# Performance work log

Measured on AMD Instinct MI355X. Metric: run time of the kernel, lower is better.

The kernel has to match this reference:

```python
import jax, jax.numpy as jnp
import numpy as np

N_NODES = 100_000
N_EDGES = 1_600_000
NFEAT = 16          # nfeature_dim
HID = 128           # hidden_dim
K = 3               # TAGConv hops in pretrained convs
N_LAYERS = 4        # pretrained n_gnn_layers (1 in->hid + 3 hid->hid)
OUT_DIM = 1


def _gcn_norm(edge_index, n):
    # PyG TAGConv: symmetric gcn_norm WITHOUT self-loops (k=0 term covers self).
    row, col = edge_index[0], edge_index[1]
    deg = jax.ops.segment_sum(jnp.ones((edge_index.shape[1],), jnp.float32), col, num_segments=n)
    dis = jnp.where(deg > 0, jax.lax.rsqrt(jnp.maximum(deg, 1.0)), 0.0)
    return dis[row] * dis[col]


def _tagconv(x, row, col, norm, ws, b, n):
    # out = sum_k (A_hat^k x) W_k + b ; ws: [K+1, in, out]
    out = x @ ws[0]
    h = x
    for k in range(1, ws.shape[0]):
        h = jax.ops.segment_sum(h[row] * norm[:, None], col, num_segments=n)
        out = out + h @ ws[k]
    return out + b


def setup_inputs() -> dict:
    key = jax.random.key(0)
    ks = jax.random.split(key, 10)
    x = jax.random.normal(ks[0], (N_NODES, NFEAT + 1), jnp.float32)
    edge_index = jax.random.randint(ks[1], (2, N_EDGES), 0, N_NODES, dtype=jnp.int64)
    # featureEmbedding: TAGConv(17 -> 16, K=1) -> 2 weight mats + bias
    fe_ws = jax.random.normal(ks[2], (2, NFEAT + 1, NFEAT), jnp.float32) * (NFEAT + 1) ** -0.5
    fe_b = jnp.zeros((NFEAT,), jnp.float32)
    # convs[0]: TAGConv(16 -> 128, K=3)
    conv0_ws = jax.random.normal(ks[3], (K + 1, NFEAT, HID), jnp.float32) * NFEAT ** -0.5
    conv0_b = jnp.zeros((HID,), jnp.float32)
    # convs[1..3]: TAGConv(128 -> 128, K=3), stacked
    conv_ws = jax.random.normal(ks[4], (N_LAYERS - 1, K + 1, HID, HID), jnp.float32) * HID ** -0.5
    conv_b = jnp.zeros((N_LAYERS - 1, HID), jnp.float32)
    fc_w = jax.random.normal(ks[5], (HID, OUT_DIM), jnp.float32) * HID ** -0.5
    fc_b = jnp.zeros((OUT_DIM,), jnp.float32)
    return {"x": x, "edge_index": edge_index, "fe_ws": fe_ws, "fe_b": fe_b,
            "conv0_ws": conv0_ws, "conv0_b": conv0_b,
            "conv_ws": conv_ws, "conv_b": conv_b, "fc_w": fc_w, "fc_b": fc_b}


def reference(x, edge_index, fe_ws, fe_b, conv0_ws, conv0_b, conv_ws, conv_b, fc_w, fc_b):
    n = x.shape[0]
    row, col = edge_index[0], edge_index[1]
    norm = _gcn_norm(edge_index, n)
    # featureEmbedding (K=1)
    h = _tagconv(x, row, col, norm, fe_ws, fe_b, n)
    # convs[0..n-2] with dropout (eval-mode identity) + ReLU
    h = _tagconv(h, row, col, norm, conv0_ws, conv0_b, n)
    h = jax.nn.relu(h)
    for i in range(conv_ws.shape[0] - 1):
        h = _tagconv(h, row, col, norm, conv_ws[i], conv_b[i], n)
        h = jax.nn.relu(h)
    # last conv: no dropout/relu
    h = _tagconv(h, row, col, norm, conv_ws[-1], conv_b[-1], n)
    return h @ fc_w + fc_b
```

## Files before the change

### kernel.cpp

```cpp
#include <hip/hip_runtime.h>

#define NN 100000
#define NE 1600000
#define SCAN_B 98

typedef _Float16 half8 __attribute__((ext_vector_type(8)));
typedef float f32x4 __attribute__((ext_vector_type(4)));
struct h2s { _Float16 x, y; };
struct h4s { _Float16 a, b, c, d; };

__global__ void k_deg(const int* __restrict__ col, int* __restrict__ degi) {
  int e = blockIdx.x * blockDim.x + threadIdx.x;
  if (e < NE) atomicAdd(&degi[col[e]], 1);
}

__global__ void k_dis(const int* __restrict__ degi, float* __restrict__ dis) {
  int i = blockIdx.x * blockDim.x + threadIdx.x;
  if (i < NN) {
    int d = degi[i];
    dis[i] = d > 0 ? rsqrtf((float)d) : 0.0f;
  }
}

__global__ void k_scan1(const int* __restrict__ degi, int* __restrict__ bsum) {
  __shared__ int red[256];
  int t = threadIdx.x;
  int base = blockIdx.x * 1024 + t * 4;
  int s = 0;
#pragma unroll
  for (int u = 0; u < 4; ++u) {
    int i = base + u;
    if (i < NN) s += degi[i];
  }
  red[t] = s;
  __syncthreads();
  for (int o = 128; o; o >>= 1) {
    if (t < o) red[t] += red[t + o];
    __syncthreads();
  }
  if (t == 0) bsum[blockIdx.x] = red[0];
}

__global__ void k_scan2(const int* __restrict__ bsum, int* __restrict__ boff,
                        int* __restrict__ off) {
  __shared__ int sh[128];
  int t = threadIdx.x;
  int v = (t < SCAN_B) ? bsum[t] : 0;
  sh[t] = v;
  __syncthreads();
  for (int o = 1; o < 128; o <<= 1) {
    int u = (t >= o) ? sh[t - o] : 0;
    __syncthreads();
    sh[t] += u;
    __syncthreads();
  }
  if (t < SCAN_B) boff[t] = sh[t] - v;
  if (t == 127) off[NN] = sh[127];
}

__global__ void k_scan3(const int* __restrict__ degi, const int* __restrict__ boff,
                        int* __restrict__ off) {
  __shared__ int red[256];
  int t = threadIdx.x;
  int base = blockIdx.x * 1024 + t * 4;
  int d[4];
  int s = 0;
#pragma unroll
  for (int u = 0; u < 4; ++u) {
    int i = base + u;
    d[u] = (i < NN) ? degi[i] : 0;
    s += d[u];
  }
  red[t] = s;
  __syncthreads();
  for (int o = 1; o < 256; o <<= 1) {
    int u2 = (t >= o) ? red[t - o] : 0;
    __syncthreads();
    red[t] += u2;
    __syncthreads();
  }
  int pre = red[t] - s + boff[blockIdx.x];
#pragma unroll
  for (int u = 0; u < 4; ++u) {
    int i = base + u;
    if (i < NN) {
      off[i] = pre;
      pre += d[u];
    }
  }
}

__global__ void k_fill(const int* __restrict__ row, const int* __restrict__ col,
                       const int* __restrict__ off, int* __restrict__ cursor,
                       int* __restrict__ src) {
  int e = blockIdx.x * blockDim.x + threadIdx.x;
  if (e < NE) {
    int c = col[e];
    int slot = off[c] + atomicAdd(&cursor[c], 1);
    src[slot] = row[e];
  }
}

__global__ void k_wh(const int* __restrict__ src, const int* __restrict__ off,
                     const float* __restrict__ dis, _Float16* __restrict__ wh) {
  int t = threadIdx.x;
  int node = blockIdx.x * 8 + (t >> 3);
  int f = t & 7;
  float dn = dis[node];
  int b = off[node], e = off[node + 1];
  for (int j = b + f; j < e; j += 8) wh[j] = (_Float16)(dis[src[j]] * dn);
}

__global__ void k_wprep(const float* __restrict__ cw, _Float16* __restrict__ wt) {
  int i = blockIdx.x * 256 + threadIdx.x;
  if (i < 12 * 16384) {
    int mat = i >> 14;
    int rem = i & 16383;
    int k = rem >> 7;
    int n = rem & 127;
    wt[(mat << 14) | (n << 7) | k] = (_Float16)cw[i];
  }
}

__global__ void k_prop16h(const h2s* __restrict__ h, const int* __restrict__ off,
                          const int* __restrict__ src, const _Float16* __restrict__ wh,
                          h2s* __restrict__ out) {
  int t = threadIdx.x;
  int node = blockIdx.x * 8 + (t >> 3);
  int f = t & 7;
  int b = off[node], e = off[node + 1];
  float ax = 0.f, ay = 0.f;
  int j = b;
  for (; j + 2 <= e; j += 2) {
    int s0 = src[j], s1 = src[j + 1];
    float w0 = (float)wh[j], w1 = (float)wh[j + 1];
    h2s v0 = h[s0 * 8 + f];
    h2s v1 = h[s1 * 8 + f];
    ax = fmaf((float)v0.x, w0, fmaf((float)v1.x, w1, ax));
    ay = fmaf((float)v0.y, w0, fmaf((float)v1.y, w1, ay));
  }
  if (j < e) {
    int s = src[j];
    float w = (float)wh[j];
    h2s v = h[s * 8 + f];
    ax = fmaf((float)v.x, w, ax);
    ay = fmaf((float)v.y, w, ay);
  }
  h2s o;
  o.x = (_Float16)ax;
  o.y = (_Float16)ay;
  unsigned bits;
  __builtin_memcpy(&bits, &o, 4);
  __builtin_nontemporal_store(bits, (unsigned*)&out[node * 8 + f]);
}

__global__ void k_prop128h(const h2s* __restrict__ h, const int* __restrict__ off,
                           const int* __restrict__ src, const _Float16* __restrict__ wh,
                           h2s* __restrict__ out) {
  int node = blockIdx.x;
  int t = threadIdx.x;
  int b = off[node], e = off[node + 1];
  float ax = 0.f, ay = 0.f;
  int j = b;
  for (; j + 8 <= e; j += 8) {
    h2s v[8];
    float w[8];
#pragma unroll
    for (int u = 0; u < 8; ++u) {
      v[u] = h[src[j + u] * 64 + t];
      w[u] = (float)wh[j + u];
    }
#pragma unroll
    for (int u = 0; u < 8; ++u) {
      ax = fmaf((float)v[u].x, w[u], ax);
      ay = fmaf((float)v[u].y, w[u], ay);
    }
  }
  for (; j < e; ++j) {
    int s = src[j];
    float w = (float)wh[j];
    h2s v = h[s * 64 + t];
    ax = fmaf((float)v.x, w, ax);
    ay = fmaf((float)v.y, w, ay);
  }
  h2s o;
  o.x = (_Float16)ax;
  o.y = (_Float16)ay;
  unsigned bits;
  __builtin_memcpy(&bits, &o, 4);
  __builtin_nontemporal_store(bits, (unsigned*)&out[node * 64 + t]);
}

template <bool RELU>
__global__ __launch_bounds__(256) void k_tag4_mfma(
    const _Float16* __restrict__ A0, const _Float16* __restrict__ A1,
    const _Float16* __restrict__ A2, const _Float16* __restrict__ A3,
    const _Float16* __restrict__ Wt, const float* __restrict__ bias,
    _Float16* __restrict__ out) {
  __shared__ _Float16 Wl[16384];
  int tid = threadIdx.x;
  int wid = tid >> 6;
  int lane = tid & 63;
  int r = lane & 15, kg = lane >> 4;
  int m0 = blockIdx.x * 128 + wid * 32;
  int row0 = min(m0 + r, NN - 1);
  int row1 = min(m0 + 16 + r, NN - 1);
  f32x4 acc0[8] = {}, acc1[8] = {};
  const _Float16* As[4] = {A0, A1, A2, A3};
#pragma unroll
  for (int s = 0; s < 4; ++s) {
    const float4* Wg = (const float4*)(Wt + (s << 14));
    __syncthreads();
#pragma unroll
    for (int u = 0; u < 8; ++u) {
      int g = tid + u * 256;
      int sg = g ^ ((g >> 4) & 7);
      *(float4*)((char*)Wl + g * 16) = Wg[sg];
    }
    __syncthreads();
    const _Float16* A = As[s];
    half8 a0[4], a1[4];
#pragma unroll
    for (int kc = 0; kc < 4; ++kc) {
      int kbase = kc * 32 + kg * 8;
      a0[kc] = *(const half8*)&A[(size_t)row0 * 128 + kbase];
      a1[kc] = *(const half8*)&A[(size_t)row1 * 128 + kbase];
    }
#pragma unroll
    for (int kc = 0; kc < 4; ++kc) {
      int kb2 = (kc * 32 + kg * 8) * 2;
#pragma unroll
      for (int nb = 0; nb < 8; ++nb) {
        int n = nb * 16 + r;
        int ba = ((n << 8) + kb2) ^ ((n & 7) << 4);
        half8 b = *(const half8*)((const char*)Wl + ba);
        acc0[nb] = __builtin_amdgcn_mfma_f32_16x16x32_f16(a0[kc], b, acc0[nb], 0, 0, 0);
        acc1[nb] = __builtin_amdgcn_mfma_f32_16x16x32_f16(a1[kc], b, acc1[nb], 0, 0, 0);
      }
    }
  }
  int ccol = lane & 15;
#pragma unroll
  for (int h = 0; h < 2; ++h) {
    int crow0 = m0 + h * 16 + kg * 4;
#pragma unroll
    for (int nb = 0; nb < 8; ++nb) {
      int col = nb * 16 + ccol;
      float bv = bias[col];
      const f32x4& av = h ? acc1[nb] : acc0[nb];
#pragma unroll
      for (int e = 0; e < 4; ++e) {
        float v = av[e] + bv;
        if (RELU) v = fmaxf(v, 0.f);
        int rr = crow0 + e;
        if (rr < NN) out[(size_t)rr * 128 + col] = (_Float16)v;
      }
    }
  }
}

__global__ __launch_bounds__(256) void k_conv0_fused(
    const _Float16* __restrict__ A0, const _Float16* __restrict__ A1,
    const _Float16* __restrict__ A2, const _Float16* __restrict__ A3,
    const float* __restrict__ W , const float* __restrict__ bias,
    _Float16* __restrict__ out) {
  __shared__ float Wl[4 * 16 * 128];
  for (int i = threadIdx.x * 4; i < 4 * 16 * 128; i += 1024)
    *(float4*)&Wl[i] = *(const float4*)&W[i];
  __syncthreads();
  int r0 = blockIdx.x * 32 + (threadIdx.x >> 5) * 4;
  int c0 = (threadIdx.x & 31) * 4;
  float acc[4][4] = {};
  const _Float16* As[4] = {A0, A1, A2, A3};
#pragma unroll
  for (int s = 0; s < 4; ++s) {
    const _Float16* A = As[s];
    const float* Ws = &Wl[s * 2048];
#pragma unroll
    for (int k = 0; k < 16; k += 4) {
      float4 w0 = *(const float4*)&Ws[(k + 0) * 128 + c0];
      float4 w1 = *(const float4*)&Ws[(k + 1) * 128 + c0];
      float4 w2 = *(const float4*)&Ws[(k + 2) * 128 + c0];
      float4 w3 = *(const float4*)&Ws[(k + 3) * 128 + c0];
#pragma unroll
      for (int i = 0; i < 4; ++i) {
        h4s a4 = *(const h4s*)&A[(r0 + i) * 16 + k];
        float ax = (float)a4.a, ay = (float)a4.b, az = (float)a4.c, aw = (float)a4.d;
        acc[i][0] = fmaf(ax, w0.x, fmaf(ay, w1.x, fmaf(az, w2.x, fmaf(aw, w3.x, acc[i][0]))));
        acc[i][1] = fmaf(ax, w0.y, fmaf(ay, w1.y, fmaf(az, w2.y, fmaf(aw, w3.y, acc[i][1]))));
        acc[i][2] = fmaf(ax, w0.z, fmaf(ay, w1.z, fmaf(az, w2.z, fmaf(aw, w3.z, acc[i][2]))));
        acc[i][3] = fmaf(ax, w0.w, fmaf(ay, w1.w, fmaf(az, w2.w, fmaf(aw, w3.w, acc[i][3]))));
      }
    }
  }
#pragma unroll
  for (int i = 0; i < 4; ++i) {
    h4s o;
    o.a = (_Float16)fmaxf(acc[i][0] + bias[c0 + 0], 0.f);
    o.b = (_Float16)fmaxf(acc[i][1] + bias[c0 + 1], 0.f);
    o.c = (_Float16)fmaxf(acc[i][2] + bias[c0 + 2], 0.f);
    o.d = (_Float16)fmaxf(acc[i][3] + bias[c0 + 3], 0.f);
    *(h4s*)&out[(size_t)(r0 + i) * 128 + c0] = o;
  }
}

template <int IN, bool ACCUM, bool BIAS>
__global__ void k_mm16h(const float* __restrict__ A, const float* __restrict__ W,
                        const float* __restrict__ bias, _Float16* __restrict__ C) {
  __shared__ float Wl[IN * 16];
  for (int i = threadIdx.x; i < IN * 16; i += 256) Wl[i] = W[i];
  __syncthreads();
  int r = blockIdx.x * 16 + (threadIdx.x >> 4);
  int c = threadIdx.x & 15;
  float acc = 0.f;
  for (int k = 0; k < IN; ++k) acc += A[r * IN + k] * Wl[k * 16 + c];
  int idx = r * 16 + c;
  if (BIAS) acc += bias[c];
  if (ACCUM) acc += (float)C[idx];
  C[idx] = (_Float16)acc;
}

__global__ void k_fc(const _Float16* __restrict__ h, const float* __restrict__ w,
                     const float* __restrict__ b, float* __restrict__ out) {
  int node = blockIdx.x;
  int t = threadIdx.x;
  float s = (float)h[node * 128 + t] * w[t] + (float)h[node * 128 + t + 64] * w[t + 64];
  for (int o = 32; o; o >>= 1) s += __shfl_down(s, o);
  if (t == 0) out[node] = s + b[0];
}

extern "C" void kernel_launch(void* const* d_in, const int* in_sizes, int n_in,
                              void* d_out, int out_size, void* d_ws, size_t ws_size,
                              hipStream_t stream) {
  const float* x = (const float*)d_in[0];
  const int* ei = (const int*)d_in[1];
  const float* fe_ws = (const float*)d_in[2];
  const float* fe_b = (const float*)d_in[3];
  const float* c0_ws = (const float*)d_in[4];
  const float* c0_b = (const float*)d_in[5];
  const float* cw = (const float*)d_in[6];
  const float* cb = (const float*)d_in[7];
  const float* fcw = (const float*)d_in[8];
  const float* fcb = (const float*)d_in[9];
  float* out = (float*)d_out;

  const int* row = ei;
  const int* colv = ei + NE;

  char* wp = (char*)d_ws;
  auto alloc = [&](size_t bytes) {
    char* p = wp;
    wp += (bytes + 511) & ~(size_t)511;
    return p;
  };
  int* degi = (int*)alloc(NN * 4);
  int* off = (int*)alloc((NN + 1) * 4);
  int* cursor = (int*)alloc(NN * 4);
  int* bsum = (int*)alloc(SCAN_B * 4);
  int* boff = (int*)alloc(SCAN_B * 4);
  float* dis = (float*)alloc(NN * 4);
  int* src = (int*)alloc((size_t)NE * 4);
  _Float16* wh = (_Float16*)alloc((size_t)NE * 2);
  _Float16* wsT = (_Float16*)alloc((size_t)12 * 16384 * 2);
  _Float16* y1h = (_Float16*)alloc((size_t)NN * 16 * 2);
  _Float16* h16 = (_Float16*)alloc((size_t)NN * 16 * 2);
  _Float16* p16b = (_Float16*)alloc((size_t)NN * 16 * 2);
  _Float16* p16c = (_Float16*)alloc((size_t)NN * 16 * 2);
  _Float16* p16d = (_Float16*)alloc((size_t)NN * 16 * 2);
  _Float16* H0 = (_Float16*)alloc((size_t)NN * 128 * 2);
  _Float16* H1 = (_Float16*)alloc((size_t)NN * 128 * 2);
  _Float16* T1 = (_Float16*)alloc((size_t)NN * 128 * 2);
  _Float16* T2 = (_Float16*)alloc((size_t)NN * 128 * 2);
  _Float16* T3 = (_Float16*)alloc((size_t)NN * 128 * 2);

  hipMemsetAsync(degi, 0, NN * 4, stream);
  hipMemsetAsync(cursor, 0, NN * 4, stream);
  k_deg<<<(NE + 255) / 256, 256, 0, stream>>>(colv, degi);
  k_dis<<<(NN + 255) / 256, 256, 0, stream>>>(degi, dis);
  k_scan1<<<SCAN_B, 256, 0, stream>>>(degi, bsum);
  k_scan2<<<1, 128, 0, stream>>>(bsum, boff, off);
  k_scan3<<<SCAN_B, 256, 0, stream>>>(degi, boff, off);
  k_fill<<<(NE + 255) / 256, 256, 0, stream>>>(row, colv, off, cursor, src);
  k_wh<<<NN / 8, 64, 0, stream>>>(src, off, dis, wh);
  k_wprep<<<768, 256, 0, stream>>>(cw, wsT);

  k_mm16h<17, false, false><<<NN / 16, 256, 0, stream>>>(x, fe_ws + 17 * 16, nullptr, y1h);
  k_prop16h<<<NN / 8, 64, 0, stream>>>((const h2s*)y1h, off, src, wh, (h2s*)h16);
  k_mm16h<17, true, true><<<NN / 16, 256, 0, stream>>>(x, fe_ws, fe_b, h16);

  k_prop16h<<<NN / 8, 64, 0, stream>>>((const h2s*)h16, off, src, wh, (h2s*)p16b);
  k_prop16h<<<NN / 8, 64, 0, stream>>>((const h2s*)p16b, off, src, wh, (h2s*)p16c);
  k_prop16h<<<NN / 8, 64, 0, stream>>>((const h2s*)p16c, off, src, wh, (h2s*)p16d);
  k_conv0_fused<<<NN / 32, 256, 0, stream>>>(h16, p16b, p16c, p16d, c0_ws, c0_b, H0);

  _Float16* hin = H0;
  _Float16* hout = H1;
  int mgrid = (NN + 127) / 128;
  for (int l = 0; l < 3; ++l) {
    k_prop128h<<<NN, 64, 0, stream>>>((const h2s*)hin, off, src, wh, (h2s*)T1);
    k_prop128h<<<NN, 64, 0, stream>>>((const h2s*)T1, off, src, wh, (h2s*)T2);
    k_prop128h<<<NN, 64, 0, stream>>>((const h2s*)T2, off, src, wh, (h2s*)T3);
    const _Float16* Wl = wsT + (size_t)l * 4 * 16384;
    const float* bl = cb + l * 128;
    if (l < 2)
      k_tag4_mfma<true><<<mgrid, 256, 0, stream>>>(hin, T1, T2, T3, Wl, bl, hout);
    else
      k_tag4_mfma<false><<<mgrid, 256, 0, stream>>>(hin, T1, T2, T3, Wl, bl, hout);
    _Float16* t = hin; hin = hout; hout = t;
  }

  k_fc<<<NN, 64, 0, stream>>>(hin, fcw, fcb, out);
}
```

Measured before the change: 997.8 us.

## Build CSR via bucketed scatter and per-block shared-memory sort

Replaces the per-edge atomic scatter into CSR slots plus a separate edge-weight kernel with a two-pass scheme. Edges are first scattered into 128-node buckets using padded per-bucket atomic counters, packing row and local column into one word. A per-bucket kernel then counting-sorts in shared memory and writes src and fp16 weights together, with a global-atomic fallback for buckets that overflow shared memory. The aim is fewer contended global atomics and more coherent writes during graph preprocessing, at the cost of an extra packed buffer and one more pass over the edges.

```diff
diff --git a/kernel.cpp b/kernel.cpp
--- a/kernel.cpp
+++ b/kernel.cpp
@@ -3,6 +3,8 @@
 #define NN 100000
 #define NE 1600000
 #define SCAN_B 98
+#define NB 782
+#define MAXB 4096
 
 typedef _Float16 half8 __attribute__((ext_vector_type(8)));
 typedef float f32x4 __attribute__((ext_vector_type(4)));
@@ -90,25 +92,75 @@
   }
 }
 
-__global__ void k_fill(const int* __restrict__ row, const int* __restrict__ col,
-                       const int* __restrict__ off, int* __restrict__ cursor,
-                       int* __restrict__ src) {
+__global__ void k_bscatter(const int* __restrict__ row, const int* __restrict__ col,
+                           const int* __restrict__ off, int* __restrict__ bcur,
+                           unsigned* __restrict__ pk) {
   int e = blockIdx.x * blockDim.x + threadIdx.x;
   if (e < NE) {
     int c = col[e];
-    int slot = off[c] + atomicAdd(&cursor[c], 1);
-    src[slot] = row[e];
-  }
-}
-
-__global__ void k_wh(const int* __restrict__ src, const int* __restrict__ off,
-                     const float* __restrict__ dis, _Float16* __restrict__ wh) {
-  int t = threadIdx.x;
-  int node = blockIdx.x * 8 + (t >> 3);
-  int f = t & 7;
-  float dn = dis[node];
-  int b = off[node], e = off[node + 1];
-  for (int j = b + f; j < e; j += 8) wh[j] = (_Float16)(dis[src[j]] * dn);
+    int b = c >> 7;
+    int slot = off[b << 7] + atomicAdd(&bcur[b * 16], 1);
+    pk[slot] = (unsigned)row[e] | ((unsigned)(c & 127) << 17);
+  }
+}
+
+__global__ __launch_bounds__(256) void k_bsort(const unsigned* __restrict__ pk,
+                                               const int* __restrict__ off,
+                                               const float* __restrict__ dis,
+                                               int* __restrict__ cursor,
+                                               int* __restrict__ src,
+                                               _Float16* __restrict__ wh) {
+  __shared__ unsigned epk[MAXB];
+  __shared__ int cnt[128];
+  __shared__ int sc[128];
+  __shared__ int cur[128];
+  __shared__ float sdis[128];
+  int b = blockIdx.x;
+  int n0 = b << 7;
+  int n1 = min(n0 + 128, NN);
+  int gb = off[n0];
+  int ge = off[n1];
+  int m = ge - gb;
+  int t = threadIdx.x;
+
+  if (m > MAXB) {
+    for (int i = t; i < m; i += 256) {
+      unsigned p = pk[gb + i];
+      int c = n0 + (int)(p >> 17);
+      int r = (int)(p & 0x1FFFFu);
+      int g = off[c] + atomicAdd(&cursor[c], 1);
+      src[g] = r;
+      wh[g] = (_Float16)(dis[r] * dis[c]);
+    }
+    return;
+  }
+
+  if (t < 128) {
+    cnt[t] = 0;
+    sdis[t] = (n0 + t < NN) ? dis[n0 + t] : 0.f;
+  }
+  for (int i = t; i < m; i += 256) epk[i] = pk[gb + i];
+  __syncthreads();
+  for (int i = t; i < m; i += 256) atomicAdd(&cnt[epk[i] >> 17], 1);
+  __syncthreads();
+  if (t < 128) sc[t] = cnt[t];
+  __syncthreads();
+  for (int o = 1; o < 128; o <<= 1) {
+    int u = (t < 128 && t >= o) ? sc[t - o] : 0;
+    __syncthreads();
+    if (t < 128) sc[t] += u;
+    __syncthreads();
+  }
+  if (t < 128) cur[t] = sc[t] - cnt[t];
+  __syncthreads();
+  for (int i = t; i < m; i += 256) {
+    unsigned p = epk[i];
+    int c = (int)(p >> 17);
+    int r = (int)(p & 0x1FFFFu);
+    int pos = gb + atomicAdd(&cur[c], 1);
+    src[pos] = r;
+    wh[pos] = (_Float16)(dis[r] * sdis[c]);
+  }
 }
 
 __global__ void k_wprep(const float* __restrict__ cw, _Float16* __restrict__ wt) {
@@ -358,8 +410,10 @@
   int* cursor = (int*)alloc(NN * 4);
   int* bsum = (int*)alloc(SCAN_B * 4);
   int* boff = (int*)alloc(SCAN_B * 4);
+  int* bcur = (int*)alloc((size_t)NB * 16 * 4);
   float* dis = (float*)alloc(NN * 4);
   int* src = (int*)alloc((size_t)NE * 4);
+  unsigned* pk = (unsigned*)alloc((size_t)NE * 4);
   _Float16* wh = (_Float16*)alloc((size_t)NE * 2);
   _Float16* wsT = (_Float16*)alloc((size_t)12 * 16384 * 2);
   _Float16* y1h = (_Float16*)alloc((size_t)NN * 16 * 2);
@@ -375,13 +429,14 @@
 
   hipMemsetAsync(degi, 0, NN * 4, stream);
   hipMemsetAsync(cursor, 0, NN * 4, stream);
+  hipMemsetAsync(bcur, 0, (size_t)NB * 16 * 4, stream);
   k_deg<<<(NE + 255) / 256, 256, 0, stream>>>(colv, degi);
   k_dis<<<(NN + 255) / 256, 256, 0, stream>>>(degi, dis);
   k_scan1<<<SCAN_B, 256, 0, stream>>>(degi, bsum);
   k_scan2<<<1, 128, 0, stream>>>(bsum, boff, off);
   k_scan3<<<SCAN_B, 256, 0, stream>>>(degi, boff, off);
-  k_fill<<<(NE + 255) / 256, 256, 0, stream>>>(row, colv, off, cursor, src);
-  k_wh<<<NN / 8, 64, 0, stream>>>(src, off, dis, wh);
+  k_bscatter<<<(NE + 255) / 256, 256, 0, stream>>>(row, colv, off, bcur, pk);
+  k_bsort<<<NB, 256, 0, stream>>>(pk, off, dis, cursor, src, wh);
   k_wprep<<<768, 256, 0, stream>>>(cw, wsT);
 
   k_mm16h<17, false, false><<<NN / 16, 256, 0, stream>>>(x, fe_ws + 17 * 16, nullptr, y1h);
```

New measurement: 991.3 us. About the same (-0.7%).
